# Kernel optimization log

Hardware: AMD Instinct MI355X
Metric: run time of the kernel (lower is better)

## Reference

```python
import jax, jax.numpy as jnp
import numpy as np

N, E, DIN, DH, DC = 50000, 1600000, 128, 128, 40
EPS = 1e-5  # BatchNorm eps


def _seg_sum(v, idx, n):
    return jax.ops.segment_sum(v, idx, num_segments=n)


def setup_inputs() -> dict:
    key = jax.random.key(0)
    ks = jax.random.split(key, 24)
    rn = lambda i, shp, s=0.05: jax.random.normal(ks[i], shp, jnp.float32) * s
    return {
        "x": jax.random.normal(ks[0], (N, DIN), jnp.float32),
        "src": jax.random.randint(ks[1], (E,), 0, N, jnp.int32),
        "dst": jax.random.randint(ks[2], (E,), 0, N, jnp.int32),
        # CoNet layer 1 (in -> hidden)
        "w11s": rn(3, (DIN, DH)), "w11n": rn(4, (DIN, DH)), "b11": jnp.zeros((DH,), jnp.float32),
        "w12": rn(5, (DIN, DH)), "b12": jnp.zeros((DH,), jnp.float32),
        "w13": rn(6, (DIN, DH)), "a13l": rn(7, (DH,)), "a13r": rn(8, (DH,)), "b13": jnp.zeros((DH,), jnp.float32),
        "cw1": jax.random.uniform(ks[9], (3,), jnp.float32, 0.5, 1.5),
        # BatchNorm1d
        "g": jnp.ones((DH,), jnp.float32), "be": jnp.zeros((DH,), jnp.float32),
        # CoNet layer 2 (hidden -> out)
        "w21s": rn(10, (DH, DC)), "w21n": rn(11, (DH, DC)), "b21": jnp.zeros((DC,), jnp.float32),
        "w22": rn(12, (DH, DC)), "b22": jnp.zeros((DC,), jnp.float32),
        "w23": rn(13, (DH, DC)), "a23l": rn(14, (DC,)), "a23r": rn(15, (DC,)), "b23": jnp.zeros((DC,), jnp.float32),
        "cw2": jax.random.uniform(ks[16], (3,), jnp.float32, 0.5, 1.5),
    }


def conet(x, src, dst, ws, wn, bs, wg, bg, wa, al, ar, ba, cw):
    """AFFN CoNet: SAGE(mean) + GCN + GAT(1 head), fused by normalized weights."""
    n = x.shape[0]
    ones = jnp.ones((src.shape[0],), x.dtype)
    indeg = _seg_sum(ones, dst, n)   # in-degree per node
    outdeg = _seg_sum(ones, src, n)  # out-degree per node

    # --- SAGEConv, mean aggregator: fc_self(x) + fc_neigh(mean_neigh(x)) ---
    nei = _seg_sum(x[src], dst, n) / jnp.maximum(indeg, 1.0)[:, None]
    x1 = x @ ws + nei @ wn + bs

    ns = jnp.maximum(outdeg, 1.0) ** -0.5
    nd = jnp.maximum(indeg, 1.0) ** -0.5
    h = _seg_sum((x * ns[:, None])[src], dst, n) * nd[:, None]
    x2 = h @ wg + bg

    # --- GATConv, 1 head ---
    f = x @ wa                       # [N, out]
    el = f @ al                      # [N]
    er = f @ ar                      # [N]
    e = jax.nn.leaky_relu(el[src] + er[dst], 0.2)  # [E]
    m = jax.ops.segment_max(e, dst, num_segments=n)
    a = jnp.exp(e - m[dst])
    s = _seg_sum(a, dst, n)
    alpha = a / jnp.maximum(s[dst], 1e-9)
    x3 = _seg_sum(alpha[:, None] * f[src], dst, n) + ba

    w = cw / jnp.sum(cw)
    return w[0] * x1 + w[1] * x2 + w[2] * x3


def reference(x, src, dst,
              w11s, w11n, b11, w12, b12, w13, a13l, a13r, b13, cw1,
              g, be,
              w21s, w21n, b21, w22, b22, w23, a23l, a23r, b23, cw2):
    h = conet(x, src, dst, w11s, w11n, b11, w12, b12, w13, a13l, a13r, b13, cw1)
    # BatchNorm1d (training-mode batch statistics)
    mu = jnp.mean(h, axis=0)
    var = jnp.var(h, axis=0)
    h = (h - mu) * jax.lax.rsqrt(var + EPS) * g + be
    h = jax.nn.relu(h)
    # dropout in eval mode: identity
    h = conet(h, src, dst, w21s, w21n, b21, w22, b22, w23, a23l, a23r, b23, cw2)
    return jax.nn.log_softmax(h, axis=1)
```

## Files before the change

kernel.cpp:

```cpp
#include <hip/hip_runtime.h>
#include <hip/hip_bf16.h>
#include <math.h>

#define DIN 128
#define DH  128
#define DC  40

#define NSTRIPE 256
#define NPAD    50176
#define H8_WORDS (NPAD / 4)

typedef unsigned short u16;
typedef unsigned int u32;
typedef unsigned char u8;
typedef __attribute__((ext_vector_type(2))) float f32x2;
typedef __attribute__((ext_vector_type(4))) float f32x4;
typedef __attribute__((ext_vector_type(8))) short bf16x8;

static __device__ __forceinline__ float bf2f(u16 u) {
    union { u32 i; float f; } v; v.i = ((u32)u) << 16; return v.f;
}
static __device__ __forceinline__ u16 f2bf(float f) {
    __hip_bfloat16 h = __float2bfloat16(f);
    union { __hip_bfloat16 h; u16 u; } v; v.h = h; return v.u;
}
static __device__ __forceinline__ u32 pack2bf(float a, float b) {
    return ((u32)f2bf(b) << 16) | (u32)f2bf(a);
}
static __device__ __forceinline__ u32 cvtpk_bf16(float a, float b) {
    u32 r;
    asm("v_cvt_pk_bf16_f32 %0, %1, %2" : "=v"(r) : "v"(a), "v"(b));
    return r;
}

static __device__ __forceinline__ u8 f2fp8(float f) {
    u32 s = (__float_as_uint(f) >> 31) << 7;
    float a = fabsf(f);
    a = fminf(a, 448.f);
    if (a < 0.015625f) {
        int q = (int)rintf(a * 512.f);
        return (u8)(s | (u32)q);
    }
    u32 x = __float_as_uint(a);
    u32 lsb = (x >> 20) & 1;
    x += 0x0007FFFF + lsb;
    u32 e = (x >> 23) - 120;
    u32 m = (x >> 20) & 7;
    return (u8)(s | (e << 3) | m);
}

#if __has_builtin(__builtin_amdgcn_cvt_pk_f32_fp8)
template<bool HI>
static __device__ __forceinline__ f32x2 fp8pk(u32 w) {
    return __builtin_amdgcn_cvt_pk_f32_fp8((int)w, HI);
}
#else
static __device__ __forceinline__ float fp8dec1(u32 byte) {
    u32 s = (byte >> 7) & 1, em = byte & 0x7F;
    float v = __uint_as_float((s << 31) | (em << 20)) * 0x1p120f;
    return v;
}
template<bool HI>
static __device__ __forceinline__ f32x2 fp8pk(u32 w) {
    u32 b0 = HI ? ((w >> 16) & 0xff) : (w & 0xff);
    u32 b1 = HI ? ((w >> 24) & 0xff) : ((w >> 8) & 0xff);
    f32x2 r; r.x = fp8dec1(b0); r.y = fp8dec1(b1); return r;
}
#endif

__global__ __launch_bounds__(256) void k_prep(
        const float* w11s, const float* w11n, const float* w12, const float* w13,
        const float* b11, const float* b12, const float* b13, const float* cw1,
        const float* w21s, const float* w21n, const float* w22, const float* w23,
        const float* b21, const float* b22, const float* b23, const float* cw2,
        const float* a13l, const float* a13r, const float* a23l, const float* a23r,
        u16* __restrict__ Wf1, u16* __restrict__ Wf2,
        float* __restrict__ bc1, float* __restrict__ bc2, float* __restrict__ vattn,
        u32* __restrict__ zq, u32* __restrict__ zh) {
    int i = blockIdx.x * 256 + threadIdx.x;
    float s1 = cw1[0] + cw1[1] + cw1[2];
    float u0 = cw1[0] / s1, u1 = cw1[1] / s1, u2 = cw1[2] / s1;
    float s2 = cw2[0] + cw2[1] + cw2[2];
    float q0 = cw2[0] / s2, q1 = cw2[1] / s2, q2 = cw2[2] / s2;
    if (i < 65536) {
        int j = i & 7, lane = (i >> 3) & 63, nt = (i >> 9) & 7, kt = i >> 12;
        int k = kt * 32 + ((lane >> 4) << 3) + j;
        int n = nt * 16 + (lane & 15);
        float v;
        if (k < 128)      v = u0 * w11s[k * 128 + n];
        else if (k < 256) v = u0 * w11n[(k - 128) * 128 + n];
        else if (k < 384) v = u1 * w12[(k - 256) * 128 + n];
        else              v = u2 * w13[(k - 384) * 128 + n];
        Wf1[i] = f2bf(v);
    } else if (i < 90112) {
        int i2 = i - 65536;
        int j = i2 & 7;
        int l2 = i2 >> 3;
        int lane = l2 & 63;
        int t2 = l2 >> 6;
        int nt = t2 % 3, kt = t2 / 3;
        int k = kt * 32 + ((lane >> 4) << 3) + j;
        int n = nt * 16 + (lane & 15);
        float v = 0.f;
        if (n < 40) {
            if (k < 128)      v = q0 * w21s[k * 40 + n];
            else if (k < 256) v = q0 * w21n[(k - 128) * 40 + n];
            else if (k < 384) v = q1 * w22[(k - 256) * 40 + n];
            else              v = q2 * w23[(k - 384) * 40 + n];
        }
        Wf2[i2] = f2bf(v);
    } else if (i < 90624) {
        int t = i - 90112;
        if (t < 128) {
            float s = 0; for (int j = 0; j < 128; ++j) s += w13[t * 128 + j] * a13l[j];
            vattn[t] = s;
        } else if (t < 256) {
            int r = t - 128; float s = 0; for (int j = 0; j < 128; ++j) s += w13[r * 128 + j] * a13r[j];
            vattn[t] = s;
        } else if (t < 384) {
            int r = t - 256; float s = 0; for (int j = 0; j < 40; ++j) s += w23[r * 40 + j] * a23l[j];
            vattn[t] = s;
        } else {
            int r = t - 384; float s = 0; for (int j = 0; j < 40; ++j) s += w23[r * 40 + j] * a23r[j];
            vattn[t] = s;
        }
    } else if (i < 90752) {
        int c = i - 90624;
        bc1[c] = u0 * b11[c] + u1 * b12[c] + u2 * b13[c];
    } else if (i < 90792) {
        int c = i - 90752;
        bc2[c] = q0 * b21[c] + q1 * b22[c] + q2 * b23[c];
    } else if (i < 90856) {
        int t = i - 90792;
        if (t < 32) zq[t] = 0u; else zh[t - 32] = 0u;
    }
}

__global__ __launch_bounds__(512) void k_hist2(const int* __restrict__ src,
        const int* __restrict__ dst,
        u8* __restrict__ partialsS, u8* __restrict__ partialsD,
        u8* __restrict__ wsrank, int E, int eps) {
    __shared__ u32 histD[H8_WORDS];
    __shared__ u32 histS[H8_WORDS];
    int stripe = blockIdx.x;
    for (int i = threadIdx.x; i < H8_WORDS; i += 512) { histD[i] = 0; histS[i] = 0; }
    __syncthreads();
    int e0 = stripe * eps;
    int e1 = e0 + eps; if (e1 > E) e1 = E;
    for (int e = e0 + threadIdx.x; e < e1; e += 512) {
        int ks = src[e];
        int kd = dst[e];
        atomicAdd(&histS[ks >> 2], 1u << ((ks & 3) * 8));
        u32 old = atomicAdd(&histD[kd >> 2], 1u << ((kd & 3) * 8));
        wsrank[e] = (u8)((old >> ((kd & 3) * 8)) & 0xff);
    }
    __syncthreads();
    u32* prowS = (u32*)(partialsS + (size_t)stripe * NPAD);
    u32* prowD = (u32*)(partialsD + (size_t)stripe * NPAD);
    for (int i = threadIdx.x; i < H8_WORDS; i += 512) { prowD[i] = histD[i]; prowS[i] = histS[i]; }
}

__global__ __launch_bounds__(256) void k_pfx2(const u8* __restrict__ partialsS,
        u8* __restrict__ partialsD,
        int* __restrict__ excl, int* __restrict__ bsum,
        float* __restrict__ ns, int n) {
    int node = blockIdx.x * 256 + threadIdx.x;
    int runS = 0;
    for (int s0 = 0; s0 < NSTRIPE; s0 += 16) {
        u8 c[16];
#pragma unroll
        for (int i = 0; i < 16; ++i) c[i] = partialsS[(size_t)(s0 + i) * NPAD + node];
#pragma unroll
        for (int i = 0; i < 16; ++i) runS += c[i];
    }
    int runD = 0;
    for (int s0 = 0; s0 < NSTRIPE; s0 += 16) {
        u8 c[16];
#pragma unroll
        for (int i = 0; i < 16; ++i) c[i] = partialsD[(size_t)(s0 + i) * NPAD + node];
#pragma unroll
        for (int i = 0; i < 16; ++i) {
            partialsD[(size_t)(s0 + i) * NPAD + node] = (u8)runD;
            runD += c[i];
        }
    }
    if (node < n) {
        int d = runS < 1 ? 1 : runS;
        ns[node] = rsqrtf((float)d);
    }
    __shared__ int sh[256];
    sh[threadIdx.x] = runD; __syncthreads();
    for (int o = 1; o < 256; o <<= 1) {
        int t = (threadIdx.x >= o) ? sh[threadIdx.x - o] : 0;
        __syncthreads(); sh[threadIdx.x] += t; __syncthreads();
    }
    excl[node] = sh[threadIdx.x] - runD;
    if (threadIdx.x == 255) bsum[blockIdx.x] = sh[255];
}

__global__ __launch_bounds__(256) void k_place2(const int* __restrict__ src,
        const int* __restrict__ dst, const int* __restrict__ rowptr,
        const u8* __restrict__ partials, const u8* __restrict__ wsrank,
        int* __restrict__ col, int E, int eps) {
    int stripe = blockIdx.x;
    const u8* prow = partials + (size_t)stripe * NPAD;
    int sub = (eps + 3) >> 2;
    int e0 = stripe * eps + blockIdx.y * sub;
    int e1 = e0 + sub;
    int cap = stripe * eps + eps; if (cap > E) cap = E;
    if (e1 > cap) e1 = cap;
    for (int e = e0 + threadIdx.x; e < e1; e += 256) {
        int d = dst[e];
        col[rowptr[d] + prow[d] + wsrank[e]] = src[e];
    }
}

__global__ __launch_bounds__(256) void k_cvt_dots(const float* __restrict__ X,
        const float* __restrict__ vl, const float* __restrict__ vr, const float* __restrict__ ns,
        const int* __restrict__ excl, const int* __restrict__ bsum,
        u16* __restrict__ Xb, u8* __restrict__ Xq,
        float2* __restrict__ elns, float* __restrict__ er,
        int* __restrict__ rowptr, int n, int E, int pb) {
    __shared__ int sh[256], shE[256];
    int t = threadIdx.x;
    int v = (t < pb) ? bsum[t] : 0;
    sh[t] = v; __syncthreads();
    for (int o = 1; o < 256; o <<= 1) {
        int u = (t >= o) ? sh[t - o] : 0;
        __syncthreads(); sh[t] += u; __syncthreads();
    }
    shE[t] = sh[t] - v;
    __syncthreads();
    if (blockIdx.x == 0 && t == 0) rowptr[n] = E;
    int w = (blockIdx.x * blockDim.x + t) >> 6;
    int lane = t & 63;
    if (w >= n) return;
    float2 xv = *(const float2*)&X[(size_t)w * 128 + lane * 2];
    *(u32*)&Xb[(size_t)w * 128 + lane * 2] = cvtpk_bf16(xv.x, xv.y);
    u16 q = (u16)f2fp8(xv.x) | ((u16)f2fp8(xv.y) << 8);
    *(u16*)&Xq[(size_t)w * 128 + lane * 2] = q;
    float2 a = *(const float2*)&vl[lane * 2];
    float2 b = *(const float2*)&vr[lane * 2];
    float dl = xv.x * a.x + xv.y * a.y;
    float dr = xv.x * b.x + xv.y * b.y;
    for (int off = 32; off; off >>= 1) {
        dl += __shfl_down(dl, off);
        dr += __shfl_down(dr, off);
    }
    if (lane == 0) {
        rowptr[w] = excl[w] + shE[w >> 8];
        elns[w] = make_float2(dl, ns[w]);
        er[w] = dr;
    }
}

__global__ __launch_bounds__(256) void k_agg(const u8* __restrict__ Xq,
        const int* __restrict__ rowptr, const int* __restrict__ colsrc,
        const float2* __restrict__ elns, const float* __restrict__ er,
        u16* __restrict__ AG, int n) {
    int wave = (blockIdx.x * blockDim.x + threadIdx.x) >> 6;
    int lane = threadIdx.x & 63;
    int g = lane >> 4, gl = lane & 15;
    int w = wave * 4 + g;
    bool act = (w < n);
    int beg = 0, end = 0;
    if (act) { beg = rowptr[w]; end = rowptr[w + 1]; }
    int k = end - beg;
    float erd = act ? er[w] : 0.f;
    int kmax = k;
    kmax = max(kmax, __shfl_xor(kmax, 16));
    kmax = max(kmax, __shfl_xor(kmax, 32));
    f32x2 aS2[4] = {}, aG2[4] = {}, aA2[4] = {};
    float ssum_l = 0.f;
    for (int c = 0; c < kmax; c += 16) {
        int cnt = k - c; cnt = cnt < 0 ? 0 : (cnt > 16 ? 16 : cnt);
        int s = n; float p = 0.f, nsl = 0.f;
        if (gl < cnt) {
            s = colsrc[beg + c + gl];
            float2 v = elns[s];
            float t = v.x + erd;
            t = t > 0.f ? t : 0.2f * t;
            p = __expf(t);
            nsl = v.y;
        }
        ssum_l += p;
        int cm = kmax - c; if (cm > 16) cm = 16;
#pragma unroll 8
        for (int t = 0; t < cm; ++t) {
            int j = (g << 4) + t;
            int sj = __shfl(s, j);
            float pj = __shfl(p, j);
            float nsj = __shfl(nsl, j);
            uint2 xq = *(const uint2*)&Xq[(size_t)sj * 128 + gl * 8];
            f32x2 xv2[4] = {fp8pk<false>(xq.x), fp8pk<true>(xq.x),
                            fp8pk<false>(xq.y), fp8pk<true>(xq.y)};
            f32x2 ns2 = {nsj, nsj}, p2 = {pj, pj};
#pragma unroll
            for (int q = 0; q < 4; ++q) {
                aS2[q] += xv2[q];
                aG2[q] += ns2 * xv2[q];
                aA2[q] += p2 * xv2[q];
            }
        }
    }
    ssum_l += __shfl_xor(ssum_l, 1);
    ssum_l += __shfl_xor(ssum_l, 2);
    ssum_l += __shfl_xor(ssum_l, 4);
    ssum_l += __shfl_xor(ssum_l, 8);
    if (!act) return;
    int kc = k < 1 ? 1 : k;
    float invk = 1.f / (float)kc;
    float ndd = rsqrtf((float)kc);
    float gi = 1.f / fmaxf(ssum_l, 1e-9f);
    u16* row = AG + (size_t)w * 384;
    uint2 oS = make_uint2(pack2bf(aS2[0][0] * invk, aS2[0][1] * invk),
                          pack2bf(aS2[1][0] * invk, aS2[1][1] * invk));
    uint2 oS2 = make_uint2(pack2bf(aS2[2][0] * invk, aS2[2][1] * invk),
                           pack2bf(aS2[3][0] * invk, aS2[3][1] * invk));
    *(uint4*)&row[gl * 8] = make_uint4(oS.x, oS.y, oS2.x, oS2.y);
    uint2 oG = make_uint2(pack2bf(aG2[0][0] * ndd, aG2[0][1] * ndd),
                          pack2bf(aG2[1][0] * ndd, aG2[1][1] * ndd));
    uint2 oG2 = make_uint2(pack2bf(aG2[2][0] * ndd, aG2[2][1] * ndd),
                           pack2bf(aG2[3][0] * ndd, aG2[3][1] * ndd));
    *(uint4*)&row[128 + gl * 8] = make_uint4(oG.x, oG.y, oG2.x, oG2.y);
    uint2 oA = make_uint2(pack2bf(aA2[0][0] * gi, aA2[0][1] * gi),
                          pack2bf(aA2[1][0] * gi, aA2[1][1] * gi));
    uint2 oA2 = make_uint2(pack2bf(aA2[2][0] * gi, aA2[2][1] * gi),
                           pack2bf(aA2[3][0] * gi, aA2[3][1] * gi));
    *(uint4*)&row[256 + gl * 8] = make_uint4(oA.x, oA.y, oA2.x, oA2.y);
}

__global__ __launch_bounds__(256) void k_gemm1(const u16* __restrict__ Xb,
        const u16* __restrict__ AG, const u16* __restrict__ Wf,
        const float* __restrict__ bias, u16* __restrict__ C,
        float* __restrict__ bnpart, int M) {
    const int NT = 8;
    int wave = threadIdx.x >> 6;
    int lane = threadIdx.x & 63;
    int m0 = blockIdx.x * 64 + wave * 16;
    int arow = m0 + (lane & 15);
    if (arow >= M) arow = M - 1;
    int kq = lane >> 4;
    f32x4 acc[NT];
#pragma unroll
    for (int t = 0; t < NT; ++t) acc[t] = (f32x4){0.f, 0.f, 0.f, 0.f};
#pragma unroll
    for (int kt = 0; kt < 16; ++kt) {
        int k0 = kt * 32 + kq * 8;
        bf16x8 a;
        if (k0 < 128) a = *(const bf16x8*)&Xb[(size_t)arow * 128 + k0];
        else          a = *(const bf16x8*)&AG[(size_t)arow * 384 + (k0 - 128)];
        const u16* wb = Wf + ((size_t)kt * NT) * 512 + lane * 8;
#pragma unroll
        for (int t = 0; t < NT; ++t) {
            bf16x8 b = *(const bf16x8*)&wb[(size_t)t * 512];
            acc[t] = __builtin_amdgcn_mfma_f32_16x16x32_bf16(a, b, acc[t], 0, 0, 0);
        }
    }
    __shared__ float sS[128], sQ[128];
    if (threadIdx.x < 128) { sS[threadIdx.x] = 0.f; sQ[threadIdx.x] = 0.f; }
    __syncthreads();
    int ccol = lane & 15;
    int rbase = m0 + kq * 4;
#pragma unroll
    for (int t = 0; t < NT; ++t) {
        int col = t * 16 + ccol;
        float bv = bias[col];
        float cs = 0.f, cq = 0.f;
#pragma unroll
        for (int r = 0; r < 4; ++r) {
            int rr = rbase + r;
            float v = acc[t][r] + bv;
            if (rr < M) {
                C[(size_t)rr * 128 + col] = f2bf(v);
                cs += v; cq += v * v;
            }
        }
        cs += __shfl_xor(cs, 16); cs += __shfl_xor(cs, 32);
        cq += __shfl_xor(cq, 16); cq += __shfl_xor(cq, 32);
        if (kq == 0) {
            atomicAdd(&sS[col], cs);
            atomicAdd(&sQ[col], cq);
        }
    }
    __syncthreads();
    if (threadIdx.x < 128) {
        bnpart[(size_t)blockIdx.x * 256 + threadIdx.x] = sS[threadIdx.x];
        bnpart[(size_t)blockIdx.x * 256 + 128 + threadIdx.x] = sQ[threadIdx.x];
    }
}

__global__ __launch_bounds__(256) void k_bn_reduce(const float* __restrict__ bnpart,
                                                   float* __restrict__ bnacc, int nb) {
    int c = blockIdx.x;
    float s = 0.f;
    for (int r = threadIdx.x; r < nb; r += 256)
        s += bnpart[(size_t)r * 256 + c];
    for (int o = 32; o; o >>= 1) s += __shfl_xor(s, o);
    __shared__ float sw[4];
    if ((threadIdx.x & 63) == 0) sw[threadIdx.x >> 6] = s;
    __syncthreads();
    if (threadIdx.x == 0) bnacc[c] = sw[0] + sw[1] + sw[2] + sw[3];
}

__global__ __launch_bounds__(256) void k_gemm2_lsm(const u16* __restrict__ Xb,
        const u16* __restrict__ AG, const u16* __restrict__ Wf,
        const float* __restrict__ bias, float* __restrict__ out, int M) {
    const int NT = 3;
    int wave = threadIdx.x >> 6;
    int lane = threadIdx.x & 63;
    int m0 = blockIdx.x * 64 + wave * 16;
    int arow = m0 + (lane & 15);
    if (arow >= M) arow = M - 1;
    int kq = lane >> 4;
    f32x4 acc[NT];
#pragma unroll
    for (int t = 0; t < NT; ++t) acc[t] = (f32x4){0.f, 0.f, 0.f, 0.f};
#pragma unroll
    for (int kt = 0; kt < 16; ++kt) {
        int k0 = kt * 32 + kq * 8;
        bf16x8 a;
        if (k0 < 128) a = *(const bf16x8*)&Xb[(size_t)arow * 128 + k0];
        else          a = *(const bf16x8*)&AG[(size_t)arow * 384 + (k0 - 128)];
        const u16* wb = Wf + ((size_t)kt * NT) * 512 + lane * 8;
#pragma unroll
        for (int t = 0; t < NT; ++t) {
            bf16x8 b = *(const bf16x8*)&wb[(size_t)t * 512];
            acc[t] = __builtin_amdgcn_mfma_f32_16x16x32_bf16(a, b, acc[t], 0, 0, 0);
        }
    }
    int ccol = lane & 15;
    int rbase = m0 + kq * 4;
    bool valid[NT];
    float bv[NT];
#pragma unroll
    for (int t = 0; t < NT; ++t) {
        int col = t * 16 + ccol;
        valid[t] = (col < 40);
        bv[t] = valid[t] ? bias[col] : 0.f;
    }
#pragma unroll
    for (int r = 0; r < 4; ++r) {
        float v[NT];
#pragma unroll
        for (int t = 0; t < NT; ++t) v[t] = valid[t] ? (acc[t][r] + bv[t]) : -INFINITY;
        float mx = fmaxf(fmaxf(v[0], v[1]), v[2]);
        for (int o = 1; o < 16; o <<= 1) mx = fmaxf(mx, __shfl_xor(mx, o));
        float se = 0.f;
#pragma unroll
        for (int t = 0; t < NT; ++t) se += valid[t] ? __expf(v[t] - mx) : 0.f;
        for (int o = 1; o < 16; o <<= 1) se += __shfl_xor(se, o);
        float lse = mx + logf(se);
        int rr = rbase + r;
        if (rr < M) {
#pragma unroll
            for (int t = 0; t < NT; ++t) {
                int col = t * 16 + ccol;
                if (valid[t]) out[(size_t)rr * 40 + col] = v[t] - lse;
            }
        }
    }
}

__global__ __launch_bounds__(256) void k_bnorm_dots(const u16* __restrict__ Hp,
        const float* __restrict__ bnacc, const float* __restrict__ g, const float* __restrict__ be,
        const float* __restrict__ vl, const float* __restrict__ vr,
        const float* __restrict__ ns,
        u16* __restrict__ H, u8* __restrict__ H8,
        float2* __restrict__ elns, float* __restrict__ er, float Nf, int n) {
    int w = (blockIdx.x * blockDim.x + threadIdx.x) >> 6;
    int lane = threadIdx.x & 63;
    if (w >= n) return;
    int c0 = lane * 2, c1 = lane * 2 + 1;
    float mu0 = bnacc[c0] / Nf, mu1 = bnacc[c1] / Nf;
    float var0 = bnacc[128 + c0] / Nf - mu0 * mu0;
    float var1 = bnacc[128 + c1] / Nf - mu1 * mu1;
    float sc0 = g[c0] * rsqrtf(var0 + 1e-5f);
    float sc1 = g[c1] * rsqrtf(var1 + 1e-5f);
    float sh0 = be[c0] - mu0 * sc0;
    float sh1 = be[c1] - mu1 * sc1;
    u32 hu = *(const u32*)&Hp[(size_t)w * 128 + lane * 2];
    float vx = bf2f((u16)hu), vy = bf2f((u16)(hu >> 16));
    float h0 = fmaxf(vx * sc0 + sh0, 0.f);
    float h1 = fmaxf(vy * sc1 + sh1, 0.f);
    *(u32*)&H[(size_t)w * 128 + lane * 2] = cvtpk_bf16(h0, h1);
    u16 q = (u16)f2fp8(h0) | ((u16)f2fp8(h1) << 8);
    *(u16*)&H8[(size_t)w * 128 + lane * 2] = q;
    float2 a = *(const float2*)&vl[lane * 2];
    float2 b = *(const float2*)&vr[lane * 2];
    float dl = h0 * a.x + h1 * a.y;
    float dr = h0 * b.x + h1 * b.y;
    for (int off = 32; off; off >>= 1) {
        dl += __shfl_down(dl, off);
        dr += __shfl_down(dr, off);
    }
    if (lane == 0) { elns[w] = make_float2(dl, ns[w]); er[w] = dr; }
}

extern "C" void kernel_launch(void* const* d_in, const int* in_sizes, int n_in,
                              void* d_out, int out_size, void* d_ws, size_t ws_size,
                              hipStream_t stream) {
    const float* x    = (const float*)d_in[0];
    const int*   src  = (const int*)d_in[1];
    const int*   dst  = (const int*)d_in[2];
    const float* w11s = (const float*)d_in[3];
    const float* w11n = (const float*)d_in[4];
    const float* b11  = (const float*)d_in[5];
    const float* w12  = (const float*)d_in[6];
    const float* b12  = (const float*)d_in[7];
    const float* w13  = (const float*)d_in[8];
    const float* a13l = (const float*)d_in[9];
    const float* a13r = (const float*)d_in[10];
    const float* b13  = (const float*)d_in[11];
    const float* cw1  = (const float*)d_in[12];
    const float* g    = (const float*)d_in[13];
    const float* be   = (const float*)d_in[14];
    const float* w21s = (const float*)d_in[15];
    const float* w21n = (const float*)d_in[16];
    const float* b21  = (const float*)d_in[17];
    const float* w22  = (const float*)d_in[18];
    const float* b22  = (const float*)d_in[19];
    const float* w23  = (const float*)d_in[20];
    const float* a23l = (const float*)d_in[21];
    const float* a23r = (const float*)d_in[22];
    const float* b23  = (const float*)d_in[23];
    const float* cw2  = (const float*)d_in[24];

    const int N = in_sizes[0] / DIN;
    const int E = in_sizes[1];

    char* ws = (char*)d_ws;
    size_t off = 0;
    auto alloc = [&](size_t bytes) { size_t o = off; off += (bytes + 255) & ~(size_t)255; return o; };
    u16*   Xb     = (u16*)(ws + alloc((size_t)N * 128 * 2));
    u8*    Xq     = (u8*)(ws + alloc((size_t)(N + 1) * 128));
    u16*   AG     = (u16*)(ws + alloc((size_t)N * 384 * 2));
    u16*   hpre   = (u16*)(ws + alloc((size_t)N * 128 * 2));
    u16*   h      = (u16*)(ws + alloc((size_t)N * 128 * 2));
    u8*    h8     = (u8*)(ws + alloc((size_t)(N + 1) * 128));
    int*   col    = (int*)(ws + alloc((size_t)E * 4));
    u8*    wsrank = (u8*)(ws + alloc((size_t)E));
    int*   rowptr = (int*)(ws + alloc((size_t)(N + 1) * 4));
    int*   excl   = (int*)(ws + alloc((size_t)NPAD * 4));
    int*   bsum   = (int*)(ws + alloc(256 * 4));
    float* ns     = (float*)(ws + alloc((size_t)N * 4));
    float2* elns  = (float2*)(ws + alloc((size_t)N * 8));
    float* er     = (float*)(ws + alloc((size_t)N * 4));
    u16*   Wf1    = (u16*)(ws + alloc((size_t)16 * 8 * 64 * 8 * 2));
    u16*   Wf2    = (u16*)(ws + alloc((size_t)16 * 3 * 64 * 8 * 2));
    float* bc1    = (float*)(ws + alloc(128 * 4));
    float* bc2    = (float*)(ws + alloc(40 * 4));
    float* vattn  = (float*)(ws + alloc(512 * 4));
    float* bnacc  = (float*)(ws + alloc(256 * 4));
    float* bnpart = (float*)(ws + alloc((size_t)((N + 63) / 64) * 256 * 4));

    u8* partialsS = (u8*)AG;
    u8* partialsD = (u8*)hpre;

    int eps = (E + NSTRIPE - 1) / NSTRIPE;
    int wb = (N * 64 + 255) / 256;
    int ab = (N + 15) / 16;
    int gb = (N + 63) / 64;
    int pb = NPAD / 256;

    k_prep<<<(90856 + 255) / 256, 256, 0, stream>>>(
        w11s, w11n, w12, w13, b11, b12, b13, cw1,
        w21s, w21n, w22, w23, b21, b22, b23, cw2,
        a13l, a13r, a23l, a23r, Wf1, Wf2, bc1, bc2, vattn,
        (u32*)(Xq + (size_t)N * 128), (u32*)(h8 + (size_t)N * 128));

    k_hist2<<<NSTRIPE, 512, 0, stream>>>(src, dst, partialsS, partialsD, wsrank, E, eps);
    k_pfx2<<<pb, 256, 0, stream>>>(partialsS, partialsD, excl, bsum, ns, N);

    k_cvt_dots<<<wb, 256, 0, stream>>>(x, vattn, vattn + 128, ns, excl, bsum,
                                       Xb, Xq, elns, er, rowptr, N, E, pb);
    {
        dim3 pg(NSTRIPE, 4);
        k_place2<<<pg, 256, 0, stream>>>(src, dst, rowptr, partialsD, wsrank, col, E, eps);
    }

    k_agg<<<ab, 256, 0, stream>>>(Xq, rowptr, col, elns, er, AG, N);
    k_gemm1<<<gb, 256, 0, stream>>>(Xb, AG, Wf1, bc1, hpre, bnpart, N);

    k_bn_reduce<<<256, 256, 0, stream>>>(bnpart, bnacc, gb);
    k_bnorm_dots<<<wb, 256, 0, stream>>>(hpre, bnacc, g, be, vattn + 256, vattn + 384, ns,
                                         h, h8, elns, er, (float)N, N);

    k_agg<<<ab, 256, 0, stream>>>(h8, rowptr, col, elns, er, AG, N);
    k_gemm2_lsm<<<gb, 256, 0, stream>>>(h, AG, Wf2, bc2, (float*)d_out, N);
}
```

Baseline: 366.2 us.

## Fuse neighbor aggregation into GEMM kernels via shared-memory tiles

The aggregation kernel and the following MFMA GEMM are merged into one 512-thread kernel per layer. Each block first aggregates its 64 rows (SAGE, GCN and GAT sums) into a padded shared-memory tile, then runs the GEMM reading the aggregated operand from LDS instead of a global N×384 bf16 buffer. This removes a large global write and read round trip and one launch per layer. In exchange it adds a large LDS footprint per block, which can lower occupancy and latency hiding in the gather phase, and layer 2 idles half its waves during the GEMM. The histogram kernel's block size also goes from 512 to 1024 threads.

```diff
diff --git a/kernel.cpp b/kernel.cpp
--- a/kernel.cpp
+++ b/kernel.cpp
@@ -9,6 +9,7 @@
 #define NSTRIPE 256
 #define NPAD    50176
 #define H8_WORDS (NPAD / 4)
+#define LROW    392
 
 typedef unsigned short u16;
 typedef unsigned int u32;
@@ -136,18 +137,18 @@
     }
 }
 
-__global__ __launch_bounds__(512) void k_hist2(const int* __restrict__ src,
+__global__ __launch_bounds__(1024) void k_hist2(const int* __restrict__ src,
         const int* __restrict__ dst,
         u8* __restrict__ partialsS, u8* __restrict__ partialsD,
         u8* __restrict__ wsrank, int E, int eps) {
     __shared__ u32 histD[H8_WORDS];
     __shared__ u32 histS[H8_WORDS];
     int stripe = blockIdx.x;
-    for (int i = threadIdx.x; i < H8_WORDS; i += 512) { histD[i] = 0; histS[i] = 0; }
+    for (int i = threadIdx.x; i < H8_WORDS; i += 1024) { histD[i] = 0; histS[i] = 0; }
     __syncthreads();
     int e0 = stripe * eps;
     int e1 = e0 + eps; if (e1 > E) e1 = E;
-    for (int e = e0 + threadIdx.x; e < e1; e += 512) {
+    for (int e = e0 + threadIdx.x; e < e1; e += 1024) {
         int ks = src[e];
         int kd = dst[e];
         atomicAdd(&histS[ks >> 2], 1u << ((ks & 3) * 8));
@@ -157,7 +158,7 @@
     __syncthreads();
     u32* prowS = (u32*)(partialsS + (size_t)stripe * NPAD);
     u32* prowD = (u32*)(partialsD + (size_t)stripe * NPAD);
-    for (int i = threadIdx.x; i < H8_WORDS; i += 512) { prowD[i] = histD[i]; prowS[i] = histS[i]; }
+    for (int i = threadIdx.x; i < H8_WORDS; i += 1024) { prowD[i] = histD[i]; prowS[i] = histS[i]; }
 }
 
 __global__ __launch_bounds__(256) void k_pfx2(const u8* __restrict__ partialsS,
@@ -254,14 +255,10 @@
     }
 }
 
-__global__ __launch_bounds__(256) void k_agg(const u8* __restrict__ Xq,
+static __device__ __forceinline__ void agg_tile(const u8* __restrict__ F,
         const int* __restrict__ rowptr, const int* __restrict__ colsrc,
         const float2* __restrict__ elns, const float* __restrict__ er,
-        u16* __restrict__ AG, int n) {
-    int wave = (blockIdx.x * blockDim.x + threadIdx.x) >> 6;
-    int lane = threadIdx.x & 63;
-    int g = lane >> 4, gl = lane & 15;
-    int w = wave * 4 + g;
+        int n, int w, int g, int gl, u16* __restrict__ dstRow) {
     bool act = (w < n);
     int beg = 0, end = 0;
     if (act) { beg = rowptr[w]; end = rowptr[w + 1]; }
@@ -291,15 +288,15 @@
             int sj = __shfl(s, j);
             float pj = __shfl(p, j);
             float nsj = __shfl(nsl, j);
-            uint2 xq = *(const uint2*)&Xq[(size_t)sj * 128 + gl * 8];
+            uint2 xq = *(const uint2*)&F[(size_t)sj * 128 + gl * 8];
             f32x2 xv2[4] = {fp8pk<false>(xq.x), fp8pk<true>(xq.x),
                             fp8pk<false>(xq.y), fp8pk<true>(xq.y)};
-            f32x2 ns2 = {nsj, nsj}, p2 = {pj, pj};
+            f32x2 ns2 = {nsj, nsj}, pw = {pj, pj};
 #pragma unroll
             for (int q = 0; q < 4; ++q) {
                 aS2[q] += xv2[q];
                 aG2[q] += ns2 * xv2[q];
-                aA2[q] += p2 * xv2[q];
+                aA2[q] += pw * xv2[q];
             }
         }
     }
@@ -307,73 +304,76 @@
     ssum_l += __shfl_xor(ssum_l, 2);
     ssum_l += __shfl_xor(ssum_l, 4);
     ssum_l += __shfl_xor(ssum_l, 8);
-    if (!act) return;
     int kc = k < 1 ? 1 : k;
     float invk = 1.f / (float)kc;
     float ndd = rsqrtf((float)kc);
     float gi = 1.f / fmaxf(ssum_l, 1e-9f);
-    u16* row = AG + (size_t)w * 384;
-    uint2 oS = make_uint2(pack2bf(aS2[0][0] * invk, aS2[0][1] * invk),
-                          pack2bf(aS2[1][0] * invk, aS2[1][1] * invk));
-    uint2 oS2 = make_uint2(pack2bf(aS2[2][0] * invk, aS2[2][1] * invk),
-                           pack2bf(aS2[3][0] * invk, aS2[3][1] * invk));
-    *(uint4*)&row[gl * 8] = make_uint4(oS.x, oS.y, oS2.x, oS2.y);
-    uint2 oG = make_uint2(pack2bf(aG2[0][0] * ndd, aG2[0][1] * ndd),
-                          pack2bf(aG2[1][0] * ndd, aG2[1][1] * ndd));
-    uint2 oG2 = make_uint2(pack2bf(aG2[2][0] * ndd, aG2[2][1] * ndd),
-                           pack2bf(aG2[3][0] * ndd, aG2[3][1] * ndd));
-    *(uint4*)&row[128 + gl * 8] = make_uint4(oG.x, oG.y, oG2.x, oG2.y);
-    uint2 oA = make_uint2(pack2bf(aA2[0][0] * gi, aA2[0][1] * gi),
-                          pack2bf(aA2[1][0] * gi, aA2[1][1] * gi));
-    uint2 oA2 = make_uint2(pack2bf(aA2[2][0] * gi, aA2[2][1] * gi),
-                           pack2bf(aA2[3][0] * gi, aA2[3][1] * gi));
-    *(uint4*)&row[256 + gl * 8] = make_uint4(oA.x, oA.y, oA2.x, oA2.y);
-}
-
-__global__ __launch_bounds__(256) void k_gemm1(const u16* __restrict__ Xb,
-        const u16* __restrict__ AG, const u16* __restrict__ Wf,
+    *(uint4*)&dstRow[gl * 8] = make_uint4(
+        pack2bf(aS2[0][0] * invk, aS2[0][1] * invk), pack2bf(aS2[1][0] * invk, aS2[1][1] * invk),
+        pack2bf(aS2[2][0] * invk, aS2[2][1] * invk), pack2bf(aS2[3][0] * invk, aS2[3][1] * invk));
+    *(uint4*)&dstRow[128 + gl * 8] = make_uint4(
+        pack2bf(aG2[0][0] * ndd, aG2[0][1] * ndd), pack2bf(aG2[1][0] * ndd, aG2[1][1] * ndd),
+        pack2bf(aG2[2][0] * ndd, aG2[2][1] * ndd), pack2bf(aG2[3][0] * ndd, aG2[3][1] * ndd));
+    *(uint4*)&dstRow[256 + gl * 8] = make_uint4(
+        pack2bf(aA2[0][0] * gi, aA2[0][1] * gi), pack2bf(aA2[1][0] * gi, aA2[1][1] * gi),
+        pack2bf(aA2[2][0] * gi, aA2[2][1] * gi), pack2bf(aA2[3][0] * gi, aA2[3][1] * gi));
+}
+
+__global__ __launch_bounds__(512) void k_aggemm1(const u8* __restrict__ Xq,
+        const int* __restrict__ rowptr, const int* __restrict__ colsrc,
+        const float2* __restrict__ elns, const float* __restrict__ er,
+        const u16* __restrict__ Xb, const u16* __restrict__ Wf,
         const float* __restrict__ bias, u16* __restrict__ C,
         float* __restrict__ bnpart, int M) {
-    const int NT = 8;
-    int wave = threadIdx.x >> 6;
-    int lane = threadIdx.x & 63;
-    int m0 = blockIdx.x * 64 + wave * 16;
-    int arow = m0 + (lane & 15);
+    __shared__ u16 AGs[64 * LROW];
+    __shared__ float sS[128], sQ[128];
+    int tid = threadIdx.x;
+    int v = tid >> 6;
+    int lane = tid & 63;
+    int g = lane >> 4, gl = lane & 15;
+    int m0 = blockIdx.x * 64;
+#pragma unroll
+    for (int it = 0; it < 2; ++it) {
+        int lw = v * 8 + it * 4 + g;
+        agg_tile(Xq, rowptr, colsrc, elns, er, M, m0 + lw, g, gl, &AGs[lw * LROW]);
+    }
+    if (tid < 128) { sS[tid] = 0.f; sQ[tid] = 0.f; }
+    __syncthreads();
+    int rq = v & 3, nh = v >> 2;
+    int lr = rq * 16 + (lane & 15);
+    int arow = m0 + lr;
     if (arow >= M) arow = M - 1;
     int kq = lane >> 4;
-    f32x4 acc[NT];
-#pragma unroll
-    for (int t = 0; t < NT; ++t) acc[t] = (f32x4){0.f, 0.f, 0.f, 0.f};
+    f32x4 acc[4];
+#pragma unroll
+    for (int t = 0; t < 4; ++t) acc[t] = (f32x4){0.f, 0.f, 0.f, 0.f};
 #pragma unroll
     for (int kt = 0; kt < 16; ++kt) {
         int k0 = kt * 32 + kq * 8;
         bf16x8 a;
         if (k0 < 128) a = *(const bf16x8*)&Xb[(size_t)arow * 128 + k0];
-        else          a = *(const bf16x8*)&AG[(size_t)arow * 384 + (k0 - 128)];
-        const u16* wb = Wf + ((size_t)kt * NT) * 512 + lane * 8;
-#pragma unroll
-        for (int t = 0; t < NT; ++t) {
+        else          a = *(const bf16x8*)&AGs[lr * LROW + (k0 - 128)];
+        const u16* wb = Wf + ((size_t)(kt * 8 + nh * 4)) * 512 + lane * 8;
+#pragma unroll
+        for (int t = 0; t < 4; ++t) {
             bf16x8 b = *(const bf16x8*)&wb[(size_t)t * 512];
             acc[t] = __builtin_amdgcn_mfma_f32_16x16x32_bf16(a, b, acc[t], 0, 0, 0);
         }
     }
-    __shared__ float sS[128], sQ[128];
-    if (threadIdx.x < 128) { sS[threadIdx.x] = 0.f; sQ[threadIdx.x] = 0.f; }
-    __syncthreads();
     int ccol = lane & 15;
-    int rbase = m0 + kq * 4;
-#pragma unroll
-    for (int t = 0; t < NT; ++t) {
-        int col = t * 16 + ccol;
+    int rbase = m0 + rq * 16 + kq * 4;
+#pragma unroll
+    for (int t = 0; t < 4; ++t) {
+        int col = (nh * 4 + t) * 16 + ccol;
         float bv = bias[col];
         float cs = 0.f, cq = 0.f;
 #pragma unroll
         for (int r = 0; r < 4; ++r) {
             int rr = rbase + r;
-            float v = acc[t][r] + bv;
+            float val = acc[t][r] + bv;
             if (rr < M) {
-                C[(size_t)rr * 128 + col] = f2bf(v);
-                cs += v; cq += v * v;
+                C[(size_t)rr * 128 + col] = f2bf(val);
+                cs += val; cq += val * val;
             }
         }
         cs += __shfl_xor(cs, 16); cs += __shfl_xor(cs, 32);
@@ -384,9 +384,9 @@
         }
     }
     __syncthreads();
-    if (threadIdx.x < 128) {
-        bnpart[(size_t)blockIdx.x * 256 + threadIdx.x] = sS[threadIdx.x];
-        bnpart[(size_t)blockIdx.x * 256 + 128 + threadIdx.x] = sQ[threadIdx.x];
+    if (tid < 128) {
+        bnpart[(size_t)blockIdx.x * 256 + tid] = sS[tid];
+        bnpart[(size_t)blockIdx.x * 256 + 128 + tid] = sQ[tid];
     }
 }
 
@@ -403,14 +403,27 @@
     if (threadIdx.x == 0) bnacc[c] = sw[0] + sw[1] + sw[2] + sw[3];
 }
 
-__global__ __launch_bounds__(256) void k_gemm2_lsm(const u16* __restrict__ Xb,
-        const u16* __restrict__ AG, const u16* __restrict__ Wf,
+__global__ __launch_bounds__(512) void k_aggemm2(const u8* __restrict__ H8,
+        const int* __restrict__ rowptr, const int* __restrict__ colsrc,
+        const float2* __restrict__ elns, const float* __restrict__ er,
+        const u16* __restrict__ Hb, const u16* __restrict__ Wf,
         const float* __restrict__ bias, float* __restrict__ out, int M) {
+    __shared__ u16 AGs[64 * LROW];
+    int tid = threadIdx.x;
+    int v = tid >> 6;
+    int lane = tid & 63;
+    int g = lane >> 4, gl = lane & 15;
+    int m0 = blockIdx.x * 64;
+#pragma unroll
+    for (int it = 0; it < 2; ++it) {
+        int lw = v * 8 + it * 4 + g;
+        agg_tile(H8, rowptr, colsrc, elns, er, M, m0 + lw, g, gl, &AGs[lw * LROW]);
+    }
+    __syncthreads();
+    if (v >= 4) return;
     const int NT = 3;
-    int wave = threadIdx.x >> 6;
-    int lane = threadIdx.x & 63;
-    int m0 = blockIdx.x * 64 + wave * 16;
-    int arow = m0 + (lane & 15);
+    int lr = v * 16 + (lane & 15);
+    int arow = m0 + lr;
     if (arow >= M) arow = M - 1;
     int kq = lane >> 4;
     f32x4 acc[NT];
@@ -420,8 +433,8 @@
     for (int kt = 0; kt < 16; ++kt) {
         int k0 = kt * 32 + kq * 8;
         bf16x8 a;
-        if (k0 < 128) a = *(const bf16x8*)&Xb[(size_t)arow * 128 + k0];
-        else          a = *(const bf16x8*)&AG[(size_t)arow * 384 + (k0 - 128)];
+        if (k0 < 128) a = *(const bf16x8*)&Hb[(size_t)arow * 128 + k0];
+        else          a = *(const bf16x8*)&AGs[lr * LROW + (k0 - 128)];
         const u16* wb = Wf + ((size_t)kt * NT) * 512 + lane * 8;
 #pragma unroll
         for (int t = 0; t < NT; ++t) {
@@ -430,7 +443,7 @@
         }
     }
     int ccol = lane & 15;
-    int rbase = m0 + kq * 4;
+    int rbase = m0 + v * 16 + kq * 4;
     bool valid[NT];
     float bv[NT];
 #pragma unroll
@@ -441,14 +454,14 @@
     }
 #pragma unroll
     for (int r = 0; r < 4; ++r) {
-        float v[NT];
-#pragma unroll
-        for (int t = 0; t < NT; ++t) v[t] = valid[t] ? (acc[t][r] + bv[t]) : -INFINITY;
-        float mx = fmaxf(fmaxf(v[0], v[1]), v[2]);
+        float vv[NT];
+#pragma unroll
+        for (int t = 0; t < NT; ++t) vv[t] = valid[t] ? (acc[t][r] + bv[t]) : -INFINITY;
+        float mx = fmaxf(fmaxf(vv[0], vv[1]), vv[2]);
         for (int o = 1; o < 16; o <<= 1) mx = fmaxf(mx, __shfl_xor(mx, o));
         float se = 0.f;
 #pragma unroll
-        for (int t = 0; t < NT; ++t) se += valid[t] ? __expf(v[t] - mx) : 0.f;
+        for (int t = 0; t < NT; ++t) se += valid[t] ? __expf(vv[t] - mx) : 0.f;
         for (int o = 1; o < 16; o <<= 1) se += __shfl_xor(se, o);
         float lse = mx + logf(se);
         int rr = rbase + r;
@@ -456,7 +469,7 @@
 #pragma unroll
             for (int t = 0; t < NT; ++t) {
                 int col = t * 16 + ccol;
-                if (valid[t]) out[(size_t)rr * 40 + col] = v[t] - lse;
+                if (valid[t]) out[(size_t)rr * 40 + col] = vv[t] - lse;
             }
         }
     }
@@ -534,7 +547,7 @@
     auto alloc = [&](size_t bytes) { size_t o = off; off += (bytes + 255) & ~(size_t)255; return o; };
     u16*   Xb     = (u16*)(ws + alloc((size_t)N * 128 * 2));
     u8*    Xq     = (u8*)(ws + alloc((size_t)(N + 1) * 128));
-    u16*   AG     = (u16*)(ws + alloc((size_t)N * 384 * 2));
+    u16*   scrA   = (u16*)(ws + alloc((size_t)N * 384 * 2));
     u16*   hpre   = (u16*)(ws + alloc((size_t)N * 128 * 2));
     u16*   h      = (u16*)(ws + alloc((size_t)N * 128 * 2));
     u8*    h8     = (u8*)(ws + alloc((size_t)(N + 1) * 128));
@@ -554,12 +567,11 @@
     float* bnacc  = (float*)(ws + alloc(256 * 4));
     float* bnpart = (float*)(ws + alloc((size_t)((N + 63) / 64) * 256 * 4));
 
-    u8* partialsS = (u8*)AG;
+    u8* partialsS = (u8*)scrA;
     u8* partialsD = (u8*)hpre;
 
     int eps = (E + NSTRIPE - 1) / NSTRIPE;
     int wb = (N * 64 + 255) / 256;
-    int ab = (N + 15) / 16;
     int gb = (N + 63) / 64;
     int pb = NPAD / 256;
 
@@ -569,7 +581,7 @@
         a13l, a13r, a23l, a23r, Wf1, Wf2, bc1, bc2, vattn,
         (u32*)(Xq + (size_t)N * 128), (u32*)(h8 + (size_t)N * 128));
 
-    k_hist2<<<NSTRIPE, 512, 0, stream>>>(src, dst, partialsS, partialsD, wsrank, E, eps);
+    k_hist2<<<NSTRIPE, 1024, 0, stream>>>(src, dst, partialsS, partialsD, wsrank, E, eps);
     k_pfx2<<<pb, 256, 0, stream>>>(partialsS, partialsD, excl, bsum, ns, N);
 
     k_cvt_dots<<<wb, 256, 0, stream>>>(x, vattn, vattn + 128, ns, excl, bsum,
@@ -579,13 +591,13 @@
         k_place2<<<pg, 256, 0, stream>>>(src, dst, rowptr, partialsD, wsrank, col, E, eps);
     }
 
-    k_agg<<<ab, 256, 0, stream>>>(Xq, rowptr, col, elns, er, AG, N);
-    k_gemm1<<<gb, 256, 0, stream>>>(Xb, AG, Wf1, bc1, hpre, bnpart, N);
+    k_aggemm1<<<gb, 512, 0, stream>>>(Xq, rowptr, col, elns, er,
+                                      Xb, Wf1, bc1, hpre, bnpart, N);
 
     k_bn_reduce<<<256, 256, 0, stream>>>(bnpart, bnacc, gb);
     k_bnorm_dots<<<wb, 256, 0, stream>>>(hpre, bnacc, g, be, vattn + 256, vattn + 384, ns,
                                          h, h8, elns, er, (float)N, N);
 
-    k_agg<<<ab, 256, 0, stream>>>(h8, rowptr, col, elns, er, AG, N);
-    k_gemm2_lsm<<<gb, 256, 0, stream>>>(h, AG, Wf2, bc2, (float*)d_out, N);
-}
+    k_aggemm2<<<gb, 512, 0, stream>>>(h8, rowptr, col, elns, er,
+                                      h, Wf2, bc2, (float*)d_out, N);
+}
```

Result: slower. 406.3 us (+10.9%).
